# Kernel optimization log

Hardware: AMD Instinct MI355X
Metric: run time of the kernel (lower is better)

The kernel has to match this reference:

```python
import jax, jax.numpy as jnp
import numpy as np
from jax import lax

WIN = 9  # window side length (default [9]*ndims in the torch module)


def _box_sum3d(x, win):
    # x: [C, 1, D, H, W]; sliding-window sum with zero padding == conv3d with
    return lax.reduce_window(
        x, jnp.array(0, x.dtype), lax.add,
        window_dimensions=(1, 1, win, win, win),
        window_strides=(1, 1, 1, 1, 1),
        padding='SAME')


def setup_inputs() -> dict:
    key = jax.random.key(0)
    k1, k2 = jax.random.split(key)
    shape = (1, 2, 192, 224, 192)  # [batch, channel, D, H, W]
    y_pred = jax.random.uniform(k1, shape, dtype=jnp.float32)
    y_true = jax.random.uniform(k2, shape, dtype=jnp.float32)
    return {"y_pred": y_pred, "y_true": y_true}


def reference(y_pred, y_true):
    # permute(1, 0, 2, 3, 4): [B, C, D, H, W] -> [C, B, D, H, W]
    Ii = jnp.transpose(y_pred, (1, 0, 2, 3, 4))
    Ji = jnp.transpose(y_true, (1, 0, 2, 3, 4))
    win_size = jnp.array(WIN ** 3, Ii.dtype)

    I_sum = _box_sum3d(Ii, WIN)
    J_sum = _box_sum3d(Ji, WIN)
    I2_sum = _box_sum3d(Ii * Ii, WIN)
    J2_sum = _box_sum3d(Ji * Ji, WIN)
    IJ_sum = _box_sum3d(Ii * Ji, WIN)

    u_I = I_sum / win_size
    u_J = J_sum / win_size

    cross = IJ_sum - u_J * I_sum - u_I * J_sum + u_I * u_J * win_size
    I_var = I2_sum - 2 * u_I * I_sum + u_I * u_I * win_size
    J_var = J2_sum - 2 * u_J * J_sum + u_J * u_J * win_size

    cc = cross * cross / (I_var * J_var + 1e-5)
    return -jnp.mean(cc)
```

## Files before the change

kernel.cpp:

```cpp
#include <hip/hip_runtime.h>
#include <hip/hip_fp16.h>


#define C2   2
#define DDIM 192
#define HDIM 224
#define WDIM 192
#define HWN  (HDIM*WDIM)
#define VOL  ((size_t)DDIM*HWN)
#define RAD  4
#define WINV (1.0f/729.0f)

#define HT1  56

__global__ __launch_bounds__(192)
void k_hwsum(const float* __restrict__ I, const float* __restrict__ J,
             __half* __restrict__ buf, int d0, int dbeg, int bufD)
{
    const int w  = threadIdx.x;
    const int d  = dbeg + blockIdx.x;
    const int h0 = blockIdx.y * HT1;
    const int c  = blockIdx.z;

    __shared__ float row[2][5][WDIM + 8];
    if (w < 8) {
        const int pos = (w < 4) ? w : (WDIM + w);
        #pragma unroll
        for (int b = 0; b < 2; ++b)
            #pragma unroll
            for (int f = 0; f < 5; ++f) row[b][f][pos] = 0.f;
    }
    __syncthreads();

    const float* Ib = I + (size_t)c*VOL + (size_t)d*HWN + w;
    const float* Jb = J + (size_t)c*VOL + (size_t)d*HWN + w;

    float ring[5][9];
    float rs[5] = {0.f,0.f,0.f,0.f,0.f};

    #pragma unroll
    for (int k = 0; k < 8; ++k) {
        const int h = h0 - RAD + k;
        float iv = 0.f, jv = 0.f;
        if (h >= 0 && h < HDIM) { iv = Ib[(size_t)h*WDIM]; jv = Jb[(size_t)h*WDIM]; }
        const float pr[5] = {iv, jv, iv*iv, jv*jv, iv*jv};
        #pragma unroll
        for (int f = 0; f < 5; ++f) { ring[f][k] = pr[f]; rs[f] += pr[f]; }
    }

    float niv = 0.f, njv = 0.f;
    {
        const int hf = h0 + RAD;
        if (hf < HDIM) { niv = Ib[(size_t)hf*WDIM]; njv = Jb[(size_t)hf*WDIM]; }
    }

    const size_t fstride = (size_t)C2*bufD*HWN;
    __half* ob = buf + ((size_t)c*bufD + (size_t)(d - d0 + RAD))*HWN + w;

    int i = 0;
    while (i < HT1) {
        #pragma unroll
        for (int p = 0; p < 9; ++p) {
            if (i < HT1) {
                const int h  = h0 + i;
                const float iv = niv, jv = njv;
                niv = 0.f; njv = 0.f;
                const int hf2 = h + 1 + RAD;
                if (i + 1 < HT1 && hf2 < HDIM) {
                    niv = Ib[(size_t)hf2*WDIM]; njv = Jb[(size_t)hf2*WDIM];
                }
                const float pr[5] = {iv, jv, iv*iv, jv*jv, iv*jv};
                float (* __restrict__ rb)[WDIM+8] = row[h & 1];
                #pragma unroll
                for (int f = 0; f < 5; ++f) {
                    rs[f] += pr[f];
                    rb[f][RAD + w] = rs[f];
                    rs[f] -= ring[f][p];
                    ring[f][(p+8)%9] = pr[f];
                }
                __syncthreads();
                #pragma unroll
                for (int f = 0; f < 5; ++f) {
                    float s = 0.f;
                    #pragma unroll
                    for (int q = 0; q < 9; ++q) s += rb[f][w + q];
                    ob[(size_t)f*fstride + (size_t)h*WDIM] = __float2half(s);
                }
                ++i;
            }
        }
    }
}

__global__ __launch_bounds__(256)
void k_dsum(const __half* __restrict__ buf, double* __restrict__ gacc,
            int d0, int bufD, int DS)
{
    const int tid = threadIdx.x;
    const int pix = blockIdx.x*256 + tid;
    const int c   = blockIdx.z;
    const int ds0 = d0 + blockIdx.y*DS;

    const size_t fstride = (size_t)C2*bufD*HWN;
    const __half* base = buf + (size_t)c*bufD*HWN + pix;

    float ring[5][9];
    float rs[5] = {0.f,0.f,0.f,0.f,0.f};
    float acc = 0.f;

    #pragma unroll
    for (int k = 0; k < 8; ++k) {
        const int dd = ds0 - RAD + k;
        float v[5] = {0.f,0.f,0.f,0.f,0.f};
        if ((unsigned)dd < (unsigned)DDIM) {
            const __half* pp = base + (size_t)(dd - d0 + RAD)*HWN;
            #pragma unroll
            for (int f = 0; f < 5; ++f) v[f] = __half2float(pp[(size_t)f*fstride]);
        }
        #pragma unroll
        for (int f = 0; f < 5; ++f) { ring[f][k] = v[f]; rs[f] += v[f]; }
    }

    int i = 0;
    while (i < DS) {
        #pragma unroll
        for (int p = 0; p < 9; ++p) {
            if (i < DS) {
                const int dd = ds0 + i + RAD;
                float v[5] = {0.f,0.f,0.f,0.f,0.f};
                if (dd < DDIM) {
                    const __half* pp = base + (size_t)(dd - d0 + RAD)*HWN;
                    #pragma unroll
                    for (int f = 0; f < 5; ++f) v[f] = __half2float(pp[(size_t)f*fstride]);
                }
                float S[5];
                #pragma unroll
                for (int f = 0; f < 5; ++f) {
                    rs[f] += v[f];
                    S[f] = rs[f];
                    rs[f] -= ring[f][p];
                    ring[f][(p+8)%9] = v[f];
                }
                const float uI    = S[0]*WINV;
                const float uJ    = S[1]*WINV;
                const float cross = S[4] - uJ*S[0];
                const float Iv    = S[2] - uI*S[0];
                const float Jv    = S[3] - uJ*S[1];
                acc += cross*cross / (Iv*Jv + 1e-5f);
                ++i;
            }
        }
    }

    __shared__ float wred[4];
    #pragma unroll
    for (int off = 32; off > 0; off >>= 1) acc += __shfl_down(acc, off);
    if ((tid & 63) == 0) wred[tid >> 6] = acc;
    __syncthreads();
    if (tid == 0) {
        const float s = wred[0] + wred[1] + wred[2] + wred[3];
        atomicAdd(gacc, (double)s);
    }
}

__global__ void k_fin(const double* __restrict__ gacc, float* __restrict__ out)
{
    out[0] = (float)(-gacc[0] / (double)((size_t)C2*DDIM*HDIM*WDIM));
}

extern "C" void kernel_launch(void* const* d_in, const int* in_sizes, int n_in,
                              void* d_out, int out_size, void* d_ws, size_t ws_size,
                              hipStream_t stream)
{
    if (n_in < 2) return;
    const float* I = (const float*)d_in[0];
    const float* J = (const float*)d_in[1];
    float* out = (float*)d_out;
    double* gacc = (double*)d_ws;
    __half* buf = (__half*)((char*)d_ws + 256);

    static const int cands[] = {192, 96, 48, 24, 12, 6, 4, 2, 1};
    int Dc = 0;
    for (int c : cands) {
        const size_t need = 256 + (size_t)5*C2*(c+8)*HWN*sizeof(__half);
        if (need <= ws_size) { Dc = c; break; }
    }
    if (Dc == 0) return;

    hipMemsetAsync(d_ws, 0, 256, stream);

    const int DS   = (Dc % 48 == 0) ? 48 : Dc;
    const int nsub = Dc / DS;
    const int bufD = Dc + 8;

    for (int d0 = 0; d0 < DDIM; d0 += Dc) {
        const int dbeg = (d0 - RAD < 0) ? 0 : d0 - RAD;
        const int dend = (d0 + Dc + RAD > DDIM) ? DDIM : d0 + Dc + RAD;
        dim3 g1(dend - dbeg, HDIM/HT1, C2);
        k_hwsum<<<g1, dim3(192,1,1), 0, stream>>>(I, J, buf, d0, dbeg, bufD);
        dim3 g2(HWN/256, nsub, C2);
        k_dsum<<<g2, dim3(256,1,1), 0, stream>>>(buf, gacc, d0, bufD, DS);
    }
    k_fin<<<1,1,0,stream>>>(gacc, out);
}
```

Measured before the change: 122.1 us.

## Process two W columns per thread and two D slices per block in H/W box-sum

The H/W box-sum kernel now has each thread handle two adjacent W columns using float2 loads and shared-memory accesses, and writes half2 outputs. The W-direction sum for the second column is derived from the first by a sliding update. Each 192-thread block covers two D slices (96 threads each), and the H tile is halved to keep the block count similar. The aim is fewer load and store instructions and fewer redundant shared-memory reads per output. The cost is more registers for float2 rings, and odd D counts are clamped to duplicate a slice, which recomputes and rewrites the same data.

```diff
diff --git a/kernel.cpp b/kernel.cpp
--- a/kernel.cpp
+++ b/kernel.cpp
@@ -11,80 +11,112 @@
 #define RAD  4
 #define WINV (1.0f/729.0f)
 
-#define HT1  56
+#define HT1  28
+#define NROW 200
 
 __global__ __launch_bounds__(192)
 void k_hwsum(const float* __restrict__ I, const float* __restrict__ J,
-             __half* __restrict__ buf, int d0, int dbeg, int bufD)
-{
-    const int w  = threadIdx.x;
-    const int d  = dbeg + blockIdx.x;
+             __half* __restrict__ buf, int d0, int dbeg, int dend, int bufD)
+{
+    const int tx = threadIdx.x;
+    const int s  = tx / 96;
+    const int p  = tx % 96;
+    const int w0 = 2 * p;
+    int d = dbeg + 2*blockIdx.x + s;
+    if (d >= dend) d = dend - 1;
     const int h0 = blockIdx.y * HT1;
     const int c  = blockIdx.z;
 
-    __shared__ float row[2][5][WDIM + 8];
-    if (w < 8) {
-        const int pos = (w < 4) ? w : (WDIM + w);
-        #pragma unroll
-        for (int b = 0; b < 2; ++b)
-            #pragma unroll
-            for (int f = 0; f < 5; ++f) row[b][f][pos] = 0.f;
+    __shared__ float row[2][2][5][NROW];
+
+    for (int t = tx; t < 2*2*5*8; t += 192) {
+        const int k    = t & 7;
+        const int rest = t >> 3;
+        const int pos  = (k < 4) ? k : (192 + k);
+        (&row[0][0][0][0])[rest*NROW + pos] = 0.f;
     }
     __syncthreads();
 
-    const float* Ib = I + (size_t)c*VOL + (size_t)d*HWN + w;
-    const float* Jb = J + (size_t)c*VOL + (size_t)d*HWN + w;
-
-    float ring[5][9];
-    float rs[5] = {0.f,0.f,0.f,0.f,0.f};
+    const float* Ib = I + (size_t)c*VOL + (size_t)d*HWN + w0;
+    const float* Jb = J + (size_t)c*VOL + (size_t)d*HWN + w0;
+
+    float2 ring[5][9];
+    float2 rs[5];
+    #pragma unroll
+    for (int f = 0; f < 5; ++f) { rs[f].x = 0.f; rs[f].y = 0.f; }
 
     #pragma unroll
     for (int k = 0; k < 8; ++k) {
         const int h = h0 - RAD + k;
-        float iv = 0.f, jv = 0.f;
-        if (h >= 0 && h < HDIM) { iv = Ib[(size_t)h*WDIM]; jv = Jb[(size_t)h*WDIM]; }
-        const float pr[5] = {iv, jv, iv*iv, jv*jv, iv*jv};
-        #pragma unroll
-        for (int f = 0; f < 5; ++f) { ring[f][k] = pr[f]; rs[f] += pr[f]; }
-    }
-
-    float niv = 0.f, njv = 0.f;
+        float2 iv = {0.f,0.f}, jv = {0.f,0.f};
+        if (h >= 0 && h < HDIM) {
+            iv = *(const float2*)(Ib + (size_t)h*WDIM);
+            jv = *(const float2*)(Jb + (size_t)h*WDIM);
+        }
+        float2 pr[5];
+        pr[0] = iv; pr[1] = jv;
+        pr[2].x = iv.x*iv.x; pr[2].y = iv.y*iv.y;
+        pr[3].x = jv.x*jv.x; pr[3].y = jv.y*jv.y;
+        pr[4].x = iv.x*jv.x; pr[4].y = iv.y*jv.y;
+        #pragma unroll
+        for (int f = 0; f < 5; ++f) {
+            ring[f][k] = pr[f];
+            rs[f].x += pr[f].x; rs[f].y += pr[f].y;
+        }
+    }
+
+    float2 niv = {0.f,0.f}, njv = {0.f,0.f};
     {
         const int hf = h0 + RAD;
-        if (hf < HDIM) { niv = Ib[(size_t)hf*WDIM]; njv = Jb[(size_t)hf*WDIM]; }
+        if (hf < HDIM) {
+            niv = *(const float2*)(Ib + (size_t)hf*WDIM);
+            njv = *(const float2*)(Jb + (size_t)hf*WDIM);
+        }
     }
 
     const size_t fstride = (size_t)C2*bufD*HWN;
-    __half* ob = buf + ((size_t)c*bufD + (size_t)(d - d0 + RAD))*HWN + w;
+    __half* ob = buf + ((size_t)c*bufD + (size_t)(d - d0 + RAD))*HWN + w0;
 
     int i = 0;
     while (i < HT1) {
         #pragma unroll
-        for (int p = 0; p < 9; ++p) {
+        for (int p9 = 0; p9 < 9; ++p9) {
             if (i < HT1) {
-                const int h  = h0 + i;
-                const float iv = niv, jv = njv;
-                niv = 0.f; njv = 0.f;
+                const int h = h0 + i;
+                const float2 iv = niv, jv = njv;
+                niv.x = 0.f; niv.y = 0.f; njv.x = 0.f; njv.y = 0.f;
                 const int hf2 = h + 1 + RAD;
                 if (i + 1 < HT1 && hf2 < HDIM) {
-                    niv = Ib[(size_t)hf2*WDIM]; njv = Jb[(size_t)hf2*WDIM];
-                }
-                const float pr[5] = {iv, jv, iv*iv, jv*jv, iv*jv};
-                float (* __restrict__ rb)[WDIM+8] = row[h & 1];
+                    niv = *(const float2*)(Ib + (size_t)hf2*WDIM);
+                    njv = *(const float2*)(Jb + (size_t)hf2*WDIM);
+                }
+                float2 pr[5];
+                pr[0] = iv; pr[1] = jv;
+                pr[2].x = iv.x*iv.x; pr[2].y = iv.y*iv.y;
+                pr[3].x = jv.x*jv.x; pr[3].y = jv.y*jv.y;
+                pr[4].x = iv.x*jv.x; pr[4].y = iv.y*jv.y;
+                float* rb = &row[s][h & 1][0][0];
                 #pragma unroll
                 for (int f = 0; f < 5; ++f) {
-                    rs[f] += pr[f];
-                    rb[f][RAD + w] = rs[f];
-                    rs[f] -= ring[f][p];
-                    ring[f][(p+8)%9] = pr[f];
+                    rs[f].x += pr[f].x; rs[f].y += pr[f].y;
+                    *(float2*)(rb + f*NROW + 4 + w0) = rs[f];
+                    rs[f].x -= ring[f][p9].x; rs[f].y -= ring[f][p9].y;
+                    ring[f][(p9+8)%9] = pr[f];
                 }
                 __syncthreads();
                 #pragma unroll
                 for (int f = 0; f < 5; ++f) {
-                    float s = 0.f;
-                    #pragma unroll
-                    for (int q = 0; q < 9; ++q) s += rb[f][w + q];
-                    ob[(size_t)f*fstride + (size_t)h*WDIM] = __float2half(s);
+                    const float* q = rb + f*NROW + w0;
+                    const float2 r0 = *(const float2*)(q + 0);
+                    const float2 r1 = *(const float2*)(q + 2);
+                    const float2 r2 = *(const float2*)(q + 4);
+                    const float2 r3 = *(const float2*)(q + 6);
+                    const float2 r4 = *(const float2*)(q + 8);
+                    const float s9 = r0.x+r0.y+r1.x+r1.y+r2.x+r2.y+r3.x+r3.y+r4.x;
+                    const float o0 = s9;
+                    const float o1 = s9 - r0.x + r4.y;
+                    *reinterpret_cast<__half2*>(ob + f*fstride + (size_t)h*WDIM)
+                        = __floats2half2_rn(o0, o1);
                 }
                 ++i;
             }
@@ -158,8 +190,8 @@
     if ((tid & 63) == 0) wred[tid >> 6] = acc;
     __syncthreads();
     if (tid == 0) {
-        const float s = wred[0] + wred[1] + wred[2] + wred[3];
-        atomicAdd(gacc, (double)s);
+        const float sum = wred[0] + wred[1] + wred[2] + wred[3];
+        atomicAdd(gacc, (double)sum);
     }
 }
 
@@ -196,8 +228,9 @@
     for (int d0 = 0; d0 < DDIM; d0 += Dc) {
         const int dbeg = (d0 - RAD < 0) ? 0 : d0 - RAD;
         const int dend = (d0 + Dc + RAD > DDIM) ? DDIM : d0 + Dc + RAD;
-        dim3 g1(dend - dbeg, HDIM/HT1, C2);
-        k_hwsum<<<g1, dim3(192,1,1), 0, stream>>>(I, J, buf, d0, dbeg, bufD);
+        const int nd   = dend - dbeg;
+        dim3 g1((nd + 1)/2, HDIM/HT1, C2);
+        k_hwsum<<<g1, dim3(192,1,1), 0, stream>>>(I, J, buf, d0, dbeg, dend, bufD);
         dim3 g2(HWN/256, nsub, C2);
         k_dsum<<<g2, dim3(256,1,1), 0, stream>>>(buf, gacc, d0, bufD, DS);
     }
```

Result: faster. 118.2 us (-3.2%).

## Restructure H/W box-sum kernel to wave-local slices with three W points per lane

Applied to the files above, without the earlier changes.

Each 64-lane wavefront of k_hwsum now handles its own D slice, with four slices per 256-thread block. Each lane owns three consecutive W positions, loaded as float3. Only raw I/J values are kept in the ring, and the squared and cross features are recomputed, which cuts register pressure. The W window sum reuses overlapping partial sums, and the block-wide __syncthreads is replaced by a wave-local LDS buffer plus an s_waitcnt, which removes barrier stalls. The trade-offs are float3 loads and 3-element half stores that coalesce less cleanly, a halved H tile that reloads more halo rows, and a reliance on wavefront lockstep for LDS correctness.

```diff
diff --git a/kernel.cpp b/kernel.cpp
--- a/kernel.cpp
+++ b/kernel.cpp
@@ -11,80 +11,114 @@
 #define RAD  4
 #define WINV (1.0f/729.0f)
 
-#define HT1  56
-
-__global__ __launch_bounds__(192)
+#define HT1  28
+#define NROW 204
+
+__global__ __launch_bounds__(256, 3)
 void k_hwsum(const float* __restrict__ I, const float* __restrict__ J,
-             __half* __restrict__ buf, int d0, int dbeg, int bufD)
-{
-    const int w  = threadIdx.x;
-    const int d  = dbeg + blockIdx.x;
+             __half* __restrict__ buf, int d0, int dbeg, int dend, int bufD)
+{
+    const int tid = threadIdx.x;
+    const int wv  = tid >> 6;
+    const int l   = tid & 63;
+    const int w0  = 3 * l;
+    int d = dbeg + 4*blockIdx.x + wv;
+    if (d >= dend) d = dend - 1;
     const int h0 = blockIdx.y * HT1;
     const int c  = blockIdx.z;
 
-    __shared__ float row[2][5][WDIM + 8];
-    if (w < 8) {
-        const int pos = (w < 4) ? w : (WDIM + w);
-        #pragma unroll
-        for (int b = 0; b < 2; ++b)
-            #pragma unroll
-            for (int f = 0; f < 5; ++f) row[b][f][pos] = 0.f;
-    }
-    __syncthreads();
-
-    const float* Ib = I + (size_t)c*VOL + (size_t)d*HWN + w;
-    const float* Jb = J + (size_t)c*VOL + (size_t)d*HWN + w;
-
-    float ring[5][9];
-    float rs[5] = {0.f,0.f,0.f,0.f,0.f};
+    __shared__ float wrow[4][5][NROW];
+
+    if (l < 4) {
+        #pragma unroll
+        for (int f = 0; f < 5; ++f) wrow[wv][f][l] = 0.f;
+    }
+    if (l < 8) {
+        #pragma unroll
+        for (int f = 0; f < 5; ++f) wrow[wv][f][196 + l] = 0.f;
+    }
+
+    const float* Ib = I + (size_t)c*VOL + (size_t)d*HWN + w0;
+    const float* Jb = J + (size_t)c*VOL + (size_t)d*HWN + w0;
+
+    float3 ringI[9], ringJ[9];
+    float3 rs[5];
+    #pragma unroll
+    for (int f = 0; f < 5; ++f) { rs[f].x = 0.f; rs[f].y = 0.f; rs[f].z = 0.f; }
 
     #pragma unroll
     for (int k = 0; k < 8; ++k) {
         const int h = h0 - RAD + k;
-        float iv = 0.f, jv = 0.f;
-        if (h >= 0 && h < HDIM) { iv = Ib[(size_t)h*WDIM]; jv = Jb[(size_t)h*WDIM]; }
-        const float pr[5] = {iv, jv, iv*iv, jv*jv, iv*jv};
-        #pragma unroll
-        for (int f = 0; f < 5; ++f) { ring[f][k] = pr[f]; rs[f] += pr[f]; }
-    }
-
-    float niv = 0.f, njv = 0.f;
+        float3 iv = {0.f,0.f,0.f}, jv = {0.f,0.f,0.f};
+        if (h >= 0 && h < HDIM) {
+            iv = *(const float3*)(Ib + (size_t)h*WDIM);
+            jv = *(const float3*)(Jb + (size_t)h*WDIM);
+        }
+        ringI[k] = iv; ringJ[k] = jv;
+        rs[0].x += iv.x;      rs[0].y += iv.y;      rs[0].z += iv.z;
+        rs[1].x += jv.x;      rs[1].y += jv.y;      rs[1].z += jv.z;
+        rs[2].x += iv.x*iv.x; rs[2].y += iv.y*iv.y; rs[2].z += iv.z*iv.z;
+        rs[3].x += jv.x*jv.x; rs[3].y += jv.y*jv.y; rs[3].z += jv.z*jv.z;
+        rs[4].x += iv.x*jv.x; rs[4].y += iv.y*jv.y; rs[4].z += iv.z*jv.z;
+    }
+
+    float3 niv = {0.f,0.f,0.f}, njv = {0.f,0.f,0.f};
     {
         const int hf = h0 + RAD;
-        if (hf < HDIM) { niv = Ib[(size_t)hf*WDIM]; njv = Jb[(size_t)hf*WDIM]; }
+        if (hf < HDIM) {
+            niv = *(const float3*)(Ib + (size_t)hf*WDIM);
+            njv = *(const float3*)(Jb + (size_t)hf*WDIM);
+        }
     }
 
     const size_t fstride = (size_t)C2*bufD*HWN;
-    __half* ob = buf + ((size_t)c*bufD + (size_t)(d - d0 + RAD))*HWN + w;
+    __half* ob = buf + ((size_t)c*bufD + (size_t)(d - d0 + RAD))*HWN + w0;
+    float* const rowp = &wrow[wv][0][0];
 
     int i = 0;
     while (i < HT1) {
         #pragma unroll
-        for (int p = 0; p < 9; ++p) {
+        for (int p9 = 0; p9 < 9; ++p9) {
             if (i < HT1) {
-                const int h  = h0 + i;
-                const float iv = niv, jv = njv;
-                niv = 0.f; njv = 0.f;
+                const int h = h0 + i;
+                const float3 iv = niv, jv = njv;
+                niv.x=0.f; niv.y=0.f; niv.z=0.f; njv.x=0.f; njv.y=0.f; njv.z=0.f;
                 const int hf2 = h + 1 + RAD;
                 if (i + 1 < HT1 && hf2 < HDIM) {
-                    niv = Ib[(size_t)hf2*WDIM]; njv = Jb[(size_t)hf2*WDIM];
-                }
-                const float pr[5] = {iv, jv, iv*iv, jv*jv, iv*jv};
-                float (* __restrict__ rb)[WDIM+8] = row[h & 1];
+                    niv = *(const float3*)(Ib + (size_t)hf2*WDIM);
+                    njv = *(const float3*)(Jb + (size_t)hf2*WDIM);
+                }
+                rs[0].x += iv.x;      rs[0].y += iv.y;      rs[0].z += iv.z;
+                rs[1].x += jv.x;      rs[1].y += jv.y;      rs[1].z += jv.z;
+                rs[2].x += iv.x*iv.x; rs[2].y += iv.y*iv.y; rs[2].z += iv.z*iv.z;
+                rs[3].x += jv.x*jv.x; rs[3].y += jv.y*jv.y; rs[3].z += jv.z*jv.z;
+                rs[4].x += iv.x*jv.x; rs[4].y += iv.y*jv.y; rs[4].z += iv.z*jv.z;
                 #pragma unroll
                 for (int f = 0; f < 5; ++f) {
-                    rs[f] += pr[f];
-                    rb[f][RAD + w] = rs[f];
-                    rs[f] -= ring[f][p];
-                    ring[f][(p+8)%9] = pr[f];
-                }
-                __syncthreads();
+                    float* q = rowp + f*NROW + 4 + w0;
+                    q[0] = rs[f].x; q[1] = rs[f].y; q[2] = rs[f].z;
+                }
+                {
+                    const float3 ri = ringI[p9], rj = ringJ[p9];
+                    rs[0].x -= ri.x;      rs[0].y -= ri.y;      rs[0].z -= ri.z;
+                    rs[1].x -= rj.x;      rs[1].y -= rj.y;      rs[1].z -= rj.z;
+                    rs[2].x -= ri.x*ri.x; rs[2].y -= ri.y*ri.y; rs[2].z -= ri.z*ri.z;
+                    rs[3].x -= rj.x*rj.x; rs[3].y -= rj.y*rj.y; rs[3].z -= rj.z*rj.z;
+                    rs[4].x -= ri.x*rj.x; rs[4].y -= ri.y*rj.y; rs[4].z -= ri.z*rj.z;
+                    ringI[(p9+8)%9] = iv; ringJ[(p9+8)%9] = jv;
+                }
+                asm volatile("s_waitcnt lgkmcnt(0)" ::: "memory");
                 #pragma unroll
                 for (int f = 0; f < 5; ++f) {
-                    float s = 0.f;
-                    #pragma unroll
-                    for (int q = 0; q < 9; ++q) s += rb[f][w + q];
-                    ob[(size_t)f*fstride + (size_t)h*WDIM] = __float2half(s);
+                    const float* q = rowp + f*NROW + 3*l;
+                    const float a0=q[0], a1=q[1], a2=q[2], a3=q[3], a4=q[4];
+                    const float a5=q[5], a6=q[6], a7=q[7], a8=q[8], a9=q[9], a10=q[10];
+                    const float o0 = ((a0+a1)+(a2+a3)) + ((a4+a5)+(a6+a7)) + a8;
+                    const float o1 = o0 - a0 + a9;
+                    const float o2 = o1 - a1 + a10;
+                    __half* pf = ob + f*fstride + (size_t)h*WDIM;
+                    *reinterpret_cast<__half2*>(pf) = __floats2half2_rn(o0, o1);
+                    pf[2] = __float2half_rn(o2);
                 }
                 ++i;
             }
@@ -158,8 +192,8 @@
     if ((tid & 63) == 0) wred[tid >> 6] = acc;
     __syncthreads();
     if (tid == 0) {
-        const float s = wred[0] + wred[1] + wred[2] + wred[3];
-        atomicAdd(gacc, (double)s);
+        const float sum = wred[0] + wred[1] + wred[2] + wred[3];
+        atomicAdd(gacc, (double)sum);
     }
 }
 
@@ -196,8 +230,9 @@
     for (int d0 = 0; d0 < DDIM; d0 += Dc) {
         const int dbeg = (d0 - RAD < 0) ? 0 : d0 - RAD;
         const int dend = (d0 + Dc + RAD > DDIM) ? DDIM : d0 + Dc + RAD;
-        dim3 g1(dend - dbeg, HDIM/HT1, C2);
-        k_hwsum<<<g1, dim3(192,1,1), 0, stream>>>(I, J, buf, d0, dbeg, bufD);
+        const int nd   = dend - dbeg;
+        dim3 g1((nd + 3)/4, HDIM/HT1, C2);
+        k_hwsum<<<g1, dim3(256,1,1), 0, stream>>>(I, J, buf, d0, dbeg, dend, bufD);
         dim3 g2(HWN/256, nsub, C2);
         k_dsum<<<g2, dim3(256,1,1), 0, stream>>>(buf, gacc, d0, bufD, DS);
     }
```

Result: no change. 123.0 us (+0.7%).
